# Performance work log

Hardware: AMD Instinct MI355X
Metric: run time of the kernel (lower is better)

The kernel has to match this reference:

```python
import jax, jax.numpy as jnp
import numpy as np

NEG_INF = -10000.0


def setup_inputs() -> dict:
    key = jax.random.key(0)
    ks = jax.random.split(key, 8)
    B, S, H, V, NU, MV = 32, 256, 768, 30522, 5, 4
    f = lambda k, shape, s=1.0: jax.random.normal(k, shape, dtype=jnp.float32) * s
    return dict(
        input_ids=jax.random.randint(ks[0], (B, S), 0, V),
        decoder_inputs=f(ks[1], (B, NU, H)),
        encoder_output=f(ks[2], (B, S, H)),
        hidden=f(ks[3], (1, B, H)),
        embed_weight=f(ks[4], (V, H), 0.02),
        gru_w_ih=f(ks[5], (3 * H, H), 0.02),
        gru_w_hh=f(ks[6], (3 * H, H), 0.02),
        gru_b_ih=jnp.zeros((3 * H,), jnp.float32),
        gru_b_hh=jnp.zeros((3 * H,), jnp.float32),
        wgen_w=f(ks[7], (1, 3 * H), 0.02),
        wgen_b=jnp.zeros((1,), jnp.float32),
        max_value=MV,
    )


def reference(input_ids, decoder_inputs, encoder_output, hidden, embed_weight,
              gru_w_ih, gru_w_hh, gru_b_ih, gru_b_hh, wgen_w, wgen_b, max_value):
    B, S = input_ids.shape
    V, H = embed_weight.shape
    mask = (input_ids == 0)                      # [B,S] pad mask
    rows = jnp.arange(B)[:, None]                # for batched scatter-add

    def gru_cell(x, h):                          # PyTorch GRU, gate order r,z,n
        gi = x @ gru_w_ih.T + gru_b_ih
        gh = h @ gru_w_hh.T + gru_b_hh
        i_r, i_z, i_n = jnp.split(gi, 3, axis=-1)
        h_r, h_z, h_n = jnp.split(gh, 3, axis=-1)
        r = jax.nn.sigmoid(i_r + h_r)
        z = jax.nn.sigmoid(i_z + h_z)
        n = jnp.tanh(i_n + r * h_n)
        return (1.0 - z) * n + z * h

    def inner(carry, _):
        w, h = carry                             # w: [B,H] current input token emb
        h = gru_cell(w, h)                       # [B,H]
        attn_e = jnp.einsum('bsh,bh->bs', encoder_output, h)
        attn_hist = jax.nn.softmax(jnp.where(mask, NEG_INF, attn_e), axis=-1)  # [B,S]
        attn_vocab = jax.nn.softmax(h @ embed_weight.T, axis=-1)               # [B,V]
        context = jnp.einsum('bs,bsh->bh', attn_hist, encoder_output)          # [B,H]
        p_gen = jax.nn.sigmoid(
            jnp.concatenate([w, h, context], axis=-1) @ wgen_w.T + wgen_b)     # [B,1]
        # pointer distribution: scatter attention mass onto vocab ids
        p_ptr = jnp.zeros((B, V), attn_vocab.dtype).at[rows, input_ids].add(attn_hist)
        p_final = p_gen * attn_vocab + (1.0 - p_gen) * p_ptr                   # [B,V]
        w_idx = jnp.argmax(p_final, axis=-1)                                   # greedy
        return (embed_weight[w_idx], h), p_final

    def outer(h, w0):                            # w0: [B,H] slot query embedding
        (_, h), p = jax.lax.scan(inner, (w0, h), None, length=max_value)
        return h, p                              # p: [max_value,B,V]

    h0 = hidden[0]                               # [B,H]
    _, outs = jax.lax.scan(outer, h0, jnp.swapaxes(decoder_inputs, 0, 1))
    # outs: [n_update, max_value, B, V] -> [B, n_update, max_value, V]
    return jnp.transpose(outs, (2, 0, 1, 3))
```

## Files before the change

kernel.cpp:

```cpp
#include <hip/hip_runtime.h>
#include <math.h>

#define B 32
#define S 256
#define H 768
#define V 30522
#define NU 5
#define MV 4
#define NEG_INF -10000.0f

#define VP 30720
#define KSPLIT 4
#define KCH 192
#define KT 32
#define VT 256
#define VPAD 260

__device__ __forceinline__ float sigm(float x){ return 1.0f/(1.0f + expf(-x)); }

__global__ __launch_bounds__(256) void gru_kernel(
    const float* __restrict__ wp, int wstride,
    const float* __restrict__ hin, float* __restrict__ hout,
    float* __restrict__ htr,
    const float* __restrict__ Wih, const float* __restrict__ Whh,
    const float* __restrict__ bih, const float* __restrict__ bhh)
{
    int wid  = blockIdx.x * 4 + (threadIdx.x >> 6);
    int lane = threadIdx.x & 63;
    int j  = wid >> 2;
    int bg = wid & 3;

    float aI0[8], aI1[8], aI2[8], aH0[8], aH1[8], aH2[8];
#pragma unroll
    for (int bb = 0; bb < 8; bb++){ aI0[bb]=aI1[bb]=aI2[bb]=aH0[bb]=aH1[bb]=aH2[bb]=0.f; }

#pragma unroll
    for (int it = 0; it < 3; it++){
        int k = it*256 + lane*4;
        float4 w0 = *(const float4*)(Wih + (size_t)(0*H + j)*H + k);
        float4 w1 = *(const float4*)(Wih + (size_t)(1*H + j)*H + k);
        float4 w2 = *(const float4*)(Wih + (size_t)(2*H + j)*H + k);
        float4 u0 = *(const float4*)(Whh + (size_t)(0*H + j)*H + k);
        float4 u1 = *(const float4*)(Whh + (size_t)(1*H + j)*H + k);
        float4 u2 = *(const float4*)(Whh + (size_t)(2*H + j)*H + k);
#pragma unroll
        for (int bb = 0; bb < 8; bb++){
            int b = bg*8 + bb;
            float4 x = *(const float4*)(wp  + (size_t)b*wstride + k);
            float4 h = *(const float4*)(hin + (size_t)b*H + k);
            aI0[bb] += w0.x*x.x + w0.y*x.y + w0.z*x.z + w0.w*x.w;
            aI1[bb] += w1.x*x.x + w1.y*x.y + w1.z*x.z + w1.w*x.w;
            aI2[bb] += w2.x*x.x + w2.y*x.y + w2.z*x.z + w2.w*x.w;
            aH0[bb] += u0.x*h.x + u0.y*h.y + u0.z*h.z + u0.w*h.w;
            aH1[bb] += u1.x*h.x + u1.y*h.y + u1.z*h.z + u1.w*h.w;
            aH2[bb] += u2.x*h.x + u2.y*h.y + u2.z*h.z + u2.w*h.w;
        }
    }
    float rRZ0[8], rRZ1[8], rIN[8], rHN[8];
#pragma unroll
    for (int bb = 0; bb < 8; bb++){
        rRZ0[bb] = aI0[bb] + aH0[bb];
        rRZ1[bb] = aI1[bb] + aH1[bb];
        rIN[bb]  = aI2[bb];
        rHN[bb]  = aH2[bb];
    }
#pragma unroll
    for (int bb = 0; bb < 8; bb++){
#pragma unroll
        for (int m = 32; m >= 1; m >>= 1){
            rRZ0[bb] += __shfl_xor(rRZ0[bb], m, 64);
            rRZ1[bb] += __shfl_xor(rRZ1[bb], m, 64);
            rIN[bb]  += __shfl_xor(rIN[bb],  m, 64);
            rHN[bb]  += __shfl_xor(rHN[bb],  m, 64);
        }
    }
    if (lane == 0){
        float brz0 = bih[j]     + bhh[j];
        float brz1 = bih[H+j]   + bhh[H+j];
        float bin_ = bih[2*H+j];
        float bhn_ = bhh[2*H+j];
#pragma unroll
        for (int bb = 0; bb < 8; bb++){
            int b = bg*8 + bb;
            float r = sigm(rRZ0[bb] + brz0);
            float z = sigm(rRZ1[bb] + brz1);
            float n = tanhf(rIN[bb] + bin_ + r*(rHN[bb] + bhn_));
            float ho = hin[(size_t)b*H + j];
            float hv = (1.0f - z)*n + z*ho;
            hout[(size_t)b*H + j] = hv;
            htr[(size_t)j*32 + b] = hv;
        }
    }
}

__global__ __launch_bounds__(256) void attn_e_kernel(
    const float* __restrict__ hb, const float* __restrict__ enc,
    float* __restrict__ attnE)
{
    int wid  = blockIdx.x * 4 + (threadIdx.x >> 6);
    int lane = threadIdx.x & 63;
    int b = wid >> 8;
    int s = wid & 255;
    const float* er = enc + ((size_t)b*S + s)*H;
    const float* hr = hb + (size_t)b*H;
    float acc = 0.f;
#pragma unroll
    for (int it = 0; it < 3; it++){
        int k = it*256 + lane*4;
        float4 e4 = *(const float4*)(er + k);
        float4 h4 = *(const float4*)(hr + k);
        acc += e4.x*h4.x + e4.y*h4.y + e4.z*h4.z + e4.w*h4.w;
    }
#pragma unroll
    for (int m = 32; m >= 1; m >>= 1) acc += __shfl_xor(acc, m, 64);
    if (lane == 0) attnE[b*S + s] = acc;
}

__global__ __launch_bounds__(256) void ctx_kernel(
    const float* __restrict__ attnE, const int* __restrict__ ids,
    const float* __restrict__ enc, float* __restrict__ attnH,
    float* __restrict__ ctx)
{
    __shared__ float ah[S];
    __shared__ float red[S];
    int b  = blockIdx.x / 3;
    int kc = blockIdx.x % 3;
    int t  = threadIdx.x;

    float e = attnE[b*S + t];
    if (ids[b*S + t] == 0) e = NEG_INF;
    red[t] = e; __syncthreads();
    for (int s = 128; s > 0; s >>= 1){ if (t < s) red[t] = fmaxf(red[t], red[t+s]); __syncthreads(); }
    float mx = red[0]; __syncthreads();
    float p = expf(e - mx);
    red[t] = p; __syncthreads();
    for (int s = 128; s > 0; s >>= 1){ if (t < s) red[t] += red[t+s]; __syncthreads(); }
    float a = p / red[0];
    ah[t] = a;
    if (kc == 0) attnH[b*S + t] = a;
    __syncthreads();

    int k = kc*256 + t;
    const float* ep = enc + (size_t)b*S*H + k;
    float acc = 0.f;
#pragma unroll 4
    for (int s = 0; s < S; s++) acc += ah[s] * ep[(size_t)s*H];
    ctx[b*H + k] = acc;
}

__global__ __launch_bounds__(256) void logits_kernel(
    const float* __restrict__ E, const float* __restrict__ htr,
    float* __restrict__ part,
    const float* __restrict__ hb, const float* __restrict__ wp, int wstride,
    const float* __restrict__ ctx, const float* __restrict__ wgw,
    const float* __restrict__ wgb, float* __restrict__ pgen)
{
    int t = threadIdx.x;

    if (blockIdx.x == 480){
        int b = t >> 3, sl = t & 7;
        float s = 0.f;
        for (int i = sl; i < 2304; i += 8){
            float xv;
            if (i < 768)        xv = wp[(size_t)b*wstride + i];
            else if (i < 1536)  xv = hb[b*H + (i - 768)];
            else                xv = ctx[b*H + (i - 1536)];
            s += xv * wgw[i];
        }
#pragma unroll
        for (int m = 4; m >= 1; m >>= 1) s += __shfl_xor(s, m, 8);
        if (sl == 0) pgen[b] = sigm(s + wgb[0]);
        return;
    }

    __shared__ float Ets[KT][VPAD];
    int vt = blockIdx.x >> 2;
    int ks = blockIdx.x & 3;
    int v0 = vt * VT;
    int k0 = ks * KCH;

    int wu = __builtin_amdgcn_readfirstlane(t >> 6);
    int l  = t & 63;
    int r  = t >> 3;
    int c4 = t & 7;

    float4 acc[8];
#pragma unroll
    for (int j = 0; j < 8; j++){ acc[j].x=0.f; acc[j].y=0.f; acc[j].z=0.f; acc[j].w=0.f; }

    for (int ph = 0; ph < KCH/KT; ph++){
        int kb = k0 + ph*KT;
        __syncthreads();
#pragma unroll
        for (int p = 0; p < 8; p++){
            int vv = v0 + p*32 + r;
            int vr = vv < V ? vv : V-1;
            float4 e4 = *(const float4*)(E + (size_t)vr*H + kb + c4*4);
            int vloc = p*32 + r;
            Ets[c4*4+0][vloc] = e4.x;
            Ets[c4*4+1][vloc] = e4.y;
            Ets[c4*4+2][vloc] = e4.z;
            Ets[c4*4+3][vloc] = e4.w;
        }
        __syncthreads();
        const float* hkp = htr + (size_t)kb*32 + 8*wu;
#pragma unroll
        for (int k = 0; k < KT; k++){
            float4 e4 = *(const float4*)(&Ets[k][l*4]);
            float h0 = hkp[k*32+0], h1 = hkp[k*32+1], h2 = hkp[k*32+2], h3 = hkp[k*32+3];
            float h4 = hkp[k*32+4], h5 = hkp[k*32+5], h6 = hkp[k*32+6], h7 = hkp[k*32+7];
            acc[0].x += h0*e4.x; acc[0].y += h0*e4.y; acc[0].z += h0*e4.z; acc[0].w += h0*e4.w;
            acc[1].x += h1*e4.x; acc[1].y += h1*e4.y; acc[1].z += h1*e4.z; acc[1].w += h1*e4.w;
            acc[2].x += h2*e4.x; acc[2].y += h2*e4.y; acc[2].z += h2*e4.z; acc[2].w += h2*e4.w;
            acc[3].x += h3*e4.x; acc[3].y += h3*e4.y; acc[3].z += h3*e4.z; acc[3].w += h3*e4.w;
            acc[4].x += h4*e4.x; acc[4].y += h4*e4.y; acc[4].z += h4*e4.z; acc[4].w += h4*e4.w;
            acc[5].x += h5*e4.x; acc[5].y += h5*e4.y; acc[5].z += h5*e4.z; acc[5].w += h5*e4.w;
            acc[6].x += h6*e4.x; acc[6].y += h6*e4.y; acc[6].z += h6*e4.z; acc[6].w += h6*e4.w;
            acc[7].x += h7*e4.x; acc[7].y += h7*e4.y; acc[7].z += h7*e4.z; acc[7].w += h7*e4.w;
        }
    }
    float* pp = part + (size_t)ks*32*VP;
    int v = v0 + l*4;
#pragma unroll
    for (int j = 0; j < 8; j++){
        int b = 8*wu + j;
        *(float4*)(pp + (size_t)b*VP + v) = acc[j];
    }
}

__global__ __launch_bounds__(1024) void vred_kernel(
    const float* __restrict__ part, float* __restrict__ vmax, float* __restrict__ vsum)
{
    __shared__ float red[1024];
    int b = blockIdx.x, t = threadIdx.x;
    float r[30]; int n = 0;
    float mx = -INFINITY;
    for (int i = t; i < V; i += 1024){
        float x = part[(size_t)b*VP + i]
                + part[(size_t)(32+b)*VP + i]
                + part[(size_t)(64+b)*VP + i]
                + part[(size_t)(96+b)*VP + i];
        r[n++] = x;
        mx = fmaxf(mx, x);
    }
    red[t] = mx; __syncthreads();
    for (int s = 512; s > 0; s >>= 1){ if (t < s) red[t] = fmaxf(red[t], red[t+s]); __syncthreads(); }
    mx = red[0]; __syncthreads();
    float sm = 0.f;
    for (int i = 0; i < n; i++) sm += expf(r[i] - mx);
    red[t] = sm; __syncthreads();
    for (int s = 512; s > 0; s >>= 1){ if (t < s) red[t] += red[t+s]; __syncthreads(); }
    if (t == 0){ vmax[b] = mx; vsum[b] = red[0]; }
}

__global__ __launch_bounds__(1024) void final_kernel(
    const float* __restrict__ part, const float* __restrict__ vmax,
    const float* __restrict__ vsum, const float* __restrict__ pgen,
    float* __restrict__ out, int u, int mm)
{
    int b = blockIdx.y;
    int v = blockIdx.x*1024 + threadIdx.x;
    if (v >= V) return;
    float x = part[(size_t)b*VP + v]
            + part[(size_t)(32+b)*VP + v]
            + part[(size_t)(64+b)*VP + v]
            + part[(size_t)(96+b)*VP + v];
    float val = pgen[b] * expf(x - vmax[b]) / vsum[b];
    out[(((size_t)b*NU + u)*MV + mm)*(size_t)V + v] = val;
}

__global__ __launch_bounds__(256) void scatter_kernel(
    const float* __restrict__ attnH, const int* __restrict__ ids,
    const float* __restrict__ pgen, float* __restrict__ out, int u, int mm)
{
    int b = blockIdx.x, s = threadIdx.x;
    int id = ids[b*S + s];
    float val = (1.0f - pgen[b]) * attnH[b*S + s];
    atomicAdd(out + (((size_t)b*NU + u)*MV + mm)*(size_t)V + id, val);
}

__global__ __launch_bounds__(1024) void argmax_kernel(
    const float* __restrict__ out, int u, int mm,
    const float* __restrict__ E, float* __restrict__ wbuf)
{
    __shared__ float rv[1024];
    __shared__ int   ri[1024];
    int b = blockIdx.x, t = threadIdx.x;
    const float* row = out + (((size_t)b*NU + u)*MV + mm)*(size_t)V;
    float bv = -INFINITY; int bi = 0;
    for (int i = t; i < V; i += 1024){
        float x = row[i];
        if (x > bv){ bv = x; bi = i; }
    }
    rv[t] = bv; ri[t] = bi; __syncthreads();
    for (int s = 512; s > 0; s >>= 1){
        if (t < s){
            if (rv[t+s] > rv[t] || (rv[t+s] == rv[t] && ri[t+s] < ri[t])){
                rv[t] = rv[t+s]; ri[t] = ri[t+s];
            }
        }
        __syncthreads();
    }
    int idx = ri[0];
    for (int k = t; k < H; k += 1024) wbuf[b*H + k] = E[(size_t)idx*H + k];
}

extern "C" void kernel_launch(void* const* d_in, const int* in_sizes, int n_in,
                              void* d_out, int out_size, void* d_ws, size_t ws_size,
                              hipStream_t stream)
{
    const int*   ids = (const int*)  d_in[0];
    const float* dec = (const float*)d_in[1];
    const float* enc = (const float*)d_in[2];
    const float* hid = (const float*)d_in[3];
    const float* E   = (const float*)d_in[4];
    const float* Wih = (const float*)d_in[5];
    const float* Whh = (const float*)d_in[6];
    const float* bih = (const float*)d_in[7];
    const float* bhh = (const float*)d_in[8];
    const float* wgw = (const float*)d_in[9];
    const float* wgb = (const float*)d_in[10];
    float* out = (float*)d_out;
    float* ws  = (float*)d_ws;

    float* wbuf    = ws;
    float* hb0     = ws + 24576;
    float* hb1     = ws + 49152;
    float* ctxb    = ws + 73728;
    float* attnE   = ws + 98304;
    float* attnH   = ws + 106496;
    float* htr     = ws + 114688;
    float* pgenb   = ws + 139264;
    float* vmaxb   = ws + 139296;
    float* vsumb   = ws + 139328;
    float* part    = ws + 139360;

    for (int u = 0; u < NU; u++){
        for (int mm = 0; mm < MV; mm++){
            int st = u*MV + mm;
            const float* wp; int wstride;
            if (mm == 0){ wp = dec + (size_t)u*H; wstride = NU*H; }
            else        { wp = wbuf;              wstride = H; }
            const float* hin = (st == 0) ? hid : ((st & 1) ? hb0 : hb1);
            float*      hout = (st & 1) ? hb1 : hb0;

            gru_kernel<<<768, 256, 0, stream>>>(wp, wstride, hin, hout, htr, Wih, Whh, bih, bhh);
            attn_e_kernel<<<2048, 256, 0, stream>>>(hout, enc, attnE);
            ctx_kernel<<<96, 256, 0, stream>>>(attnE, ids, enc, attnH, ctxb);
            logits_kernel<<<481, 256, 0, stream>>>(E, htr, part, hout, wp, wstride, ctxb, wgw, wgb, pgenb);
            vred_kernel<<<32, 1024, 0, stream>>>(part, vmaxb, vsumb);
            final_kernel<<<dim3(30, 32), 1024, 0, stream>>>(part, vmaxb, vsumb, pgenb, out, u, mm);
            scatter_kernel<<<32, 256, 0, stream>>>(attnH, ids, pgenb, out, u, mm);
            if (mm != MV-1)
                argmax_kernel<<<32, 1024, 0, stream>>>(out, u, mm, E, wbuf);
        }
    }
}
```

Measured before the change: 3.417 ms.

## Fuse softmax, scatter and argmax into one kernel; retile logits GEMV

Replaces the vocab reduction, final softmax write, pointer scatter and argmax kernels with one per-row kernel that keeps logits in registers. This avoids re-reading the partial logits and saves several launches per step. The logits kernel moves to 128-wide vocab tiles, stages h in shared memory and computes four batches per thread, doubling the block count. The fused kernel runs only 32 blocks for the output write and argmax, which may limit parallelism.

```diff
diff --git a/kernel.cpp b/kernel.cpp
--- a/kernel.cpp
+++ b/kernel.cpp
@@ -10,11 +10,11 @@
 #define NEG_INF -10000.0f
 
 #define VP 30720
+#define NT 239
+#define VT 128
 #define KSPLIT 4
 #define KCH 192
 #define KT 32
-#define VT 256
-#define VPAD 260
 
 __device__ __forceinline__ float sigm(float x){ return 1.0f/(1.0f + expf(-x)); }
 
@@ -157,7 +157,7 @@
 {
     int t = threadIdx.x;
 
-    if (blockIdx.x == 480){
+    if (blockIdx.x == NT*4){
         int b = t >> 3, sl = t & 7;
         float s = 0.f;
         for (int i = sl; i < 2304; i += 8){
@@ -173,130 +173,135 @@
         return;
     }
 
-    __shared__ float Ets[KT][VPAD];
+    __shared__ float Ets[KT][VT];
+    __shared__ float Hs[KCH][32];
+
     int vt = blockIdx.x >> 2;
     int ks = blockIdx.x & 3;
     int v0 = vt * VT;
     int k0 = ks * KCH;
 
-    int wu = __builtin_amdgcn_readfirstlane(t >> 6);
+#pragma unroll
+    for (int j = 0; j < 6; j++){
+        int idx = t + 256*j;
+        float4 hv = *(const float4*)(htr + (size_t)k0*32 + (size_t)idx*4);
+        *(float4*)((float*)Hs + (size_t)idx*4) = hv;
+    }
+
+    int w  = t >> 6;
     int l  = t & 63;
-    int r  = t >> 3;
-    int c4 = t & 7;
-
-    float4 acc[8];
-#pragma unroll
-    for (int j = 0; j < 8; j++){ acc[j].x=0.f; acc[j].y=0.f; acc[j].z=0.f; acc[j].w=0.f; }
+    int vq = l & 31;
+    int bh = l >> 5;
+    int kq = t & 7;
+    int sr = t >> 3;
+
+    float4 acc[4];
+#pragma unroll
+    for (int j = 0; j < 4; j++){ acc[j].x=0.f; acc[j].y=0.f; acc[j].z=0.f; acc[j].w=0.f; }
 
     for (int ph = 0; ph < KCH/KT; ph++){
         int kb = k0 + ph*KT;
         __syncthreads();
 #pragma unroll
-        for (int p = 0; p < 8; p++){
-            int vv = v0 + p*32 + r;
-            int vr = vv < V ? vv : V-1;
-            float4 e4 = *(const float4*)(E + (size_t)vr*H + kb + c4*4);
-            int vloc = p*32 + r;
-            Ets[c4*4+0][vloc] = e4.x;
-            Ets[c4*4+1][vloc] = e4.y;
-            Ets[c4*4+2][vloc] = e4.z;
-            Ets[c4*4+3][vloc] = e4.w;
+        for (int i = 0; i < 4; i++){
+            int v = sr + 32*i;
+            int vr = v0 + v; if (vr >= V) vr = V-1;
+            float4 e4 = *(const float4*)(E + (size_t)vr*H + kb + 4*kq);
+            Ets[4*kq+0][v] = e4.x;
+            Ets[4*kq+1][v] = e4.y;
+            Ets[4*kq+2][v] = e4.z;
+            Ets[4*kq+3][v] = e4.w;
         }
         __syncthreads();
-        const float* hkp = htr + (size_t)kb*32 + 8*wu;
-#pragma unroll
+        int hbase = 8*w + 4*bh;
+#pragma unroll 4
         for (int k = 0; k < KT; k++){
-            float4 e4 = *(const float4*)(&Ets[k][l*4]);
-            float h0 = hkp[k*32+0], h1 = hkp[k*32+1], h2 = hkp[k*32+2], h3 = hkp[k*32+3];
-            float h4 = hkp[k*32+4], h5 = hkp[k*32+5], h6 = hkp[k*32+6], h7 = hkp[k*32+7];
-            acc[0].x += h0*e4.x; acc[0].y += h0*e4.y; acc[0].z += h0*e4.z; acc[0].w += h0*e4.w;
-            acc[1].x += h1*e4.x; acc[1].y += h1*e4.y; acc[1].z += h1*e4.z; acc[1].w += h1*e4.w;
-            acc[2].x += h2*e4.x; acc[2].y += h2*e4.y; acc[2].z += h2*e4.z; acc[2].w += h2*e4.w;
-            acc[3].x += h3*e4.x; acc[3].y += h3*e4.y; acc[3].z += h3*e4.z; acc[3].w += h3*e4.w;
-            acc[4].x += h4*e4.x; acc[4].y += h4*e4.y; acc[4].z += h4*e4.z; acc[4].w += h4*e4.w;
-            acc[5].x += h5*e4.x; acc[5].y += h5*e4.y; acc[5].z += h5*e4.z; acc[5].w += h5*e4.w;
-            acc[6].x += h6*e4.x; acc[6].y += h6*e4.y; acc[6].z += h6*e4.z; acc[6].w += h6*e4.w;
-            acc[7].x += h7*e4.x; acc[7].y += h7*e4.y; acc[7].z += h7*e4.z; acc[7].w += h7*e4.w;
+            float4 e4 = *(const float4*)(&Ets[k][4*vq]);
+            float4 h4 = *(const float4*)(&Hs[ph*KT + k][hbase]);
+            acc[0].x += h4.x*e4.x; acc[0].y += h4.x*e4.y; acc[0].z += h4.x*e4.z; acc[0].w += h4.x*e4.w;
+            acc[1].x += h4.y*e4.x; acc[1].y += h4.y*e4.y; acc[1].z += h4.y*e4.z; acc[1].w += h4.y*e4.w;
+            acc[2].x += h4.z*e4.x; acc[2].y += h4.z*e4.y; acc[2].z += h4.z*e4.z; acc[2].w += h4.z*e4.w;
+            acc[3].x += h4.w*e4.x; acc[3].y += h4.w*e4.y; acc[3].z += h4.w*e4.z; acc[3].w += h4.w*e4.w;
         }
     }
     float* pp = part + (size_t)ks*32*VP;
-    int v = v0 + l*4;
-#pragma unroll
-    for (int j = 0; j < 8; j++){
-        int b = 8*wu + j;
+    int v = v0 + 4*vq;
+#pragma unroll
+    for (int j = 0; j < 4; j++){
+        int b = 8*w + 4*bh + j;
         *(float4*)(pp + (size_t)b*VP + v) = acc[j];
     }
 }
 
-__global__ __launch_bounds__(1024) void vred_kernel(
-    const float* __restrict__ part, float* __restrict__ vmax, float* __restrict__ vsum)
+__global__ __launch_bounds__(1024) void softmax_fused_kernel(
+    const float* __restrict__ part, const float* __restrict__ pgen,
+    const float* __restrict__ attnH, const int* __restrict__ ids,
+    float* __restrict__ out, const float* __restrict__ E,
+    float* __restrict__ wbuf, int u, int mm)
 {
     __shared__ float red[1024];
+    __shared__ int   ri[1024];
     int b = blockIdx.x, t = threadIdx.x;
-    float r[30]; int n = 0;
+
+    float r[30];
     float mx = -INFINITY;
-    for (int i = t; i < V; i += 1024){
-        float x = part[(size_t)b*VP + i]
-                + part[(size_t)(32+b)*VP + i]
-                + part[(size_t)(64+b)*VP + i]
-                + part[(size_t)(96+b)*VP + i];
-        r[n++] = x;
+#pragma unroll
+    for (int i = 0; i < 30; i++){
+        int v = t + 1024*i;
+        float x = -INFINITY;
+        if (v < V){
+            x = part[(size_t)b*VP + v]
+              + part[(size_t)(32+b)*VP + v]
+              + part[(size_t)(64+b)*VP + v]
+              + part[(size_t)(96+b)*VP + v];
+        }
+        r[i] = x;
         mx = fmaxf(mx, x);
     }
     red[t] = mx; __syncthreads();
     for (int s = 512; s > 0; s >>= 1){ if (t < s) red[t] = fmaxf(red[t], red[t+s]); __syncthreads(); }
     mx = red[0]; __syncthreads();
+
     float sm = 0.f;
-    for (int i = 0; i < n; i++) sm += expf(r[i] - mx);
+#pragma unroll
+    for (int i = 0; i < 30; i++){
+        if (t + 1024*i < V) sm += expf(r[i] - mx);
+    }
     red[t] = sm; __syncthreads();
     for (int s = 512; s > 0; s >>= 1){ if (t < s) red[t] += red[t+s]; __syncthreads(); }
-    if (t == 0){ vmax[b] = mx; vsum[b] = red[0]; }
-}
-
-__global__ __launch_bounds__(1024) void final_kernel(
-    const float* __restrict__ part, const float* __restrict__ vmax,
-    const float* __restrict__ vsum, const float* __restrict__ pgen,
-    float* __restrict__ out, int u, int mm)
-{
-    int b = blockIdx.y;
-    int v = blockIdx.x*1024 + threadIdx.x;
-    if (v >= V) return;
-    float x = part[(size_t)b*VP + v]
-            + part[(size_t)(32+b)*VP + v]
-            + part[(size_t)(64+b)*VP + v]
-            + part[(size_t)(96+b)*VP + v];
-    float val = pgen[b] * expf(x - vmax[b]) / vsum[b];
-    out[(((size_t)b*NU + u)*MV + mm)*(size_t)V + v] = val;
-}
-
-__global__ __launch_bounds__(256) void scatter_kernel(
-    const float* __restrict__ attnH, const int* __restrict__ ids,
-    const float* __restrict__ pgen, float* __restrict__ out, int u, int mm)
-{
-    int b = blockIdx.x, s = threadIdx.x;
-    int id = ids[b*S + s];
-    float val = (1.0f - pgen[b]) * attnH[b*S + s];
-    atomicAdd(out + (((size_t)b*NU + u)*MV + mm)*(size_t)V + id, val);
-}
-
-__global__ __launch_bounds__(1024) void argmax_kernel(
-    const float* __restrict__ out, int u, int mm,
-    const float* __restrict__ E, float* __restrict__ wbuf)
-{
-    __shared__ float rv[1024];
-    __shared__ int   ri[1024];
-    int b = blockIdx.x, t = threadIdx.x;
-    const float* row = out + (((size_t)b*NU + u)*MV + mm)*(size_t)V;
+    float sum = red[0]; __syncthreads();
+
+    float pg  = pgen[b];
+    float scl = pg / sum;
+    float* orow = out + (((size_t)b*NU + u)*MV + mm)*(size_t)V;
+#pragma unroll
+    for (int i = 0; i < 30; i++){
+        int v = t + 1024*i;
+        if (v < V) orow[v] = expf(r[i] - mx) * scl;
+    }
+    __threadfence();
+    __syncthreads();
+    if (t < S){
+        int id = ids[b*S + t];
+        atomicAdd(orow + id, (1.0f - pg) * attnH[b*S + t]);
+    }
+    __threadfence();
+    __syncthreads();
+
     float bv = -INFINITY; int bi = 0;
-    for (int i = t; i < V; i += 1024){
-        float x = row[i];
-        if (x > bv){ bv = x; bi = i; }
-    }
-    rv[t] = bv; ri[t] = bi; __syncthreads();
+#pragma unroll
+    for (int i = 0; i < 30; i++){
+        int v = t + 1024*i;
+        if (v < V){
+            float x = orow[v];
+            if (x > bv){ bv = x; bi = v; }
+        }
+    }
+    red[t] = bv; ri[t] = bi; __syncthreads();
     for (int s = 512; s > 0; s >>= 1){
         if (t < s){
-            if (rv[t+s] > rv[t] || (rv[t+s] == rv[t] && ri[t+s] < ri[t])){
-                rv[t] = rv[t+s]; ri[t] = ri[t+s];
+            if (red[t+s] > red[t] || (red[t+s] == red[t] && ri[t+s] < ri[t])){
+                red[t] = red[t+s]; ri[t] = ri[t+s];
             }
         }
         __syncthreads();
@@ -331,8 +336,6 @@
     float* attnH   = ws + 106496;
     float* htr     = ws + 114688;
     float* pgenb   = ws + 139264;
-    float* vmaxb   = ws + 139296;
-    float* vsumb   = ws + 139328;
     float* part    = ws + 139360;
 
     for (int u = 0; u < NU; u++){
@@ -347,12 +350,8 @@
             gru_kernel<<<768, 256, 0, stream>>>(wp, wstride, hin, hout, htr, Wih, Whh, bih, bhh);
             attn_e_kernel<<<2048, 256, 0, stream>>>(hout, enc, attnE);
             ctx_kernel<<<96, 256, 0, stream>>>(attnE, ids, enc, attnH, ctxb);
-            logits_kernel<<<481, 256, 0, stream>>>(E, htr, part, hout, wp, wstride, ctxb, wgw, wgb, pgenb);
-            vred_kernel<<<32, 1024, 0, stream>>>(part, vmaxb, vsumb);
-            final_kernel<<<dim3(30, 32), 1024, 0, stream>>>(part, vmaxb, vsumb, pgenb, out, u, mm);
-            scatter_kernel<<<32, 256, 0, stream>>>(attnH, ids, pgenb, out, u, mm);
-            if (mm != MV-1)
-                argmax_kernel<<<32, 1024, 0, stream>>>(out, u, mm, E, wbuf);
-        }
-    }
-}
+            logits_kernel<<<NT*4+1, 256, 0, stream>>>(E, htr, part, hout, wp, wstride, ctxb, wgw, wgb, pgenb);
+            softmax_fused_kernel<<<32, 1024, 0, stream>>>(part, pgenb, attnH, ids, out, E, wbuf, u, mm);
+        }
+    }
+}
```

Result: slower. 3.823 ms (+11.9%).

## Restructure vocab logits with 6-way K-split, prefetch, and fused softmax+scatter

Applied to the files above, without the earlier changes.

The logits kernel now splits K six ways (720 blocks), stages the hidden-state slice in shared memory, and register-prefetches the next embedding tile while computing the current one. The vocab reduction is split into 8 chunks per batch row, producing partial max/sum and a reduced logit buffer. The final kernel merges the partial softmax stats, writes float4 outputs, and performs the pointer scatter-add itself, which removes a separate kernel launch. These changes aim to raise parallelism and overlap global loads with FMA work. The cost is more partial-sum traffic and an extra intermediate buffer.

```diff
diff --git a/kernel.cpp b/kernel.cpp
--- a/kernel.cpp
+++ b/kernel.cpp
@@ -10,11 +10,12 @@
 #define NEG_INF -10000.0f
 
 #define VP 30720
-#define KSPLIT 4
-#define KCH 192
-#define KT 32
+#define VTILES 120
 #define VT 256
-#define VPAD 260
+#define KSPL 6
+#define KCH 128
+#define KT 16
+#define NPH (KCH/KT)
 
 __device__ __forceinline__ float sigm(float x){ return 1.0f/(1.0f + expf(-x)); }
 
@@ -157,7 +158,7 @@
 {
     int t = threadIdx.x;
 
-    if (blockIdx.x == 480){
+    if (blockIdx.x == VTILES*KSPL){
         int b = t >> 3, sl = t & 7;
         float s = 0.f;
         for (int i = sl; i < 2304; i += 8){
@@ -173,110 +174,152 @@
         return;
     }
 
-    __shared__ float Ets[KT][VPAD];
-    int vt = blockIdx.x >> 2;
-    int ks = blockIdx.x & 3;
+    __shared__ float Ets[KT][VT];
+    __shared__ float Hs[KCH][32];
+
+    int vt = blockIdx.x / KSPL;
+    int ks = blockIdx.x % KSPL;
     int v0 = vt * VT;
     int k0 = ks * KCH;
 
-    int wu = __builtin_amdgcn_readfirstlane(t >> 6);
+    {
+        const float4* src = (const float4*)(htr + (size_t)k0*32);
+        float4* dst = (float4*)&Hs[0][0];
+#pragma unroll
+        for (int i = 0; i < 4; i++) dst[t + 256*i] = src[t + 256*i];
+    }
+
+    int q  = t & 3;
+    int vs = t >> 2;
+    int w  = t >> 6;
     int l  = t & 63;
-    int r  = t >> 3;
-    int c4 = t & 7;
+
+    float4 pre[4];
+#pragma unroll
+    for (int a = 0; a < 4; a++){
+        int vr = v0 + vs + 64*a; if (vr >= V) vr = V-1;
+        pre[a] = *(const float4*)(E + (size_t)vr*H + k0 + 4*q);
+    }
 
     float4 acc[8];
 #pragma unroll
     for (int j = 0; j < 8; j++){ acc[j].x=0.f; acc[j].y=0.f; acc[j].z=0.f; acc[j].w=0.f; }
 
-    for (int ph = 0; ph < KCH/KT; ph++){
-        int kb = k0 + ph*KT;
+    for (int ph = 0; ph < NPH; ph++){
         __syncthreads();
 #pragma unroll
-        for (int p = 0; p < 8; p++){
-            int vv = v0 + p*32 + r;
-            int vr = vv < V ? vv : V-1;
-            float4 e4 = *(const float4*)(E + (size_t)vr*H + kb + c4*4);
-            int vloc = p*32 + r;
-            Ets[c4*4+0][vloc] = e4.x;
-            Ets[c4*4+1][vloc] = e4.y;
-            Ets[c4*4+2][vloc] = e4.z;
-            Ets[c4*4+3][vloc] = e4.w;
+        for (int a = 0; a < 4; a++){
+            int vloc = vs + 64*a;
+            Ets[4*q+0][vloc] = pre[a].x;
+            Ets[4*q+1][vloc] = pre[a].y;
+            Ets[4*q+2][vloc] = pre[a].z;
+            Ets[4*q+3][vloc] = pre[a].w;
         }
         __syncthreads();
-        const float* hkp = htr + (size_t)kb*32 + 8*wu;
+        if (ph + 1 < NPH){
+            int kn = k0 + (ph+1)*KT;
+#pragma unroll
+            for (int a = 0; a < 4; a++){
+                int vr = v0 + vs + 64*a; if (vr >= V) vr = V-1;
+                pre[a] = *(const float4*)(E + (size_t)vr*H + kn + 4*q);
+            }
+        }
 #pragma unroll
         for (int k = 0; k < KT; k++){
-            float4 e4 = *(const float4*)(&Ets[k][l*4]);
-            float h0 = hkp[k*32+0], h1 = hkp[k*32+1], h2 = hkp[k*32+2], h3 = hkp[k*32+3];
-            float h4 = hkp[k*32+4], h5 = hkp[k*32+5], h6 = hkp[k*32+6], h7 = hkp[k*32+7];
-            acc[0].x += h0*e4.x; acc[0].y += h0*e4.y; acc[0].z += h0*e4.z; acc[0].w += h0*e4.w;
-            acc[1].x += h1*e4.x; acc[1].y += h1*e4.y; acc[1].z += h1*e4.z; acc[1].w += h1*e4.w;
-            acc[2].x += h2*e4.x; acc[2].y += h2*e4.y; acc[2].z += h2*e4.z; acc[2].w += h2*e4.w;
-            acc[3].x += h3*e4.x; acc[3].y += h3*e4.y; acc[3].z += h3*e4.z; acc[3].w += h3*e4.w;
-            acc[4].x += h4*e4.x; acc[4].y += h4*e4.y; acc[4].z += h4*e4.z; acc[4].w += h4*e4.w;
-            acc[5].x += h5*e4.x; acc[5].y += h5*e4.y; acc[5].z += h5*e4.z; acc[5].w += h5*e4.w;
-            acc[6].x += h6*e4.x; acc[6].y += h6*e4.y; acc[6].z += h6*e4.z; acc[6].w += h6*e4.w;
-            acc[7].x += h7*e4.x; acc[7].y += h7*e4.y; acc[7].z += h7*e4.z; acc[7].w += h7*e4.w;
+            float4 e4 = *(const float4*)(&Ets[k][4*l]);
+            const float* hp = &Hs[ph*KT + k][8*w];
+            float4 hA = *(const float4*)(hp);
+            float4 hB = *(const float4*)(hp + 4);
+            acc[0].x += hA.x*e4.x; acc[0].y += hA.x*e4.y; acc[0].z += hA.x*e4.z; acc[0].w += hA.x*e4.w;
+            acc[1].x += hA.y*e4.x; acc[1].y += hA.y*e4.y; acc[1].z += hA.y*e4.z; acc[1].w += hA.y*e4.w;
+            acc[2].x += hA.z*e4.x; acc[2].y += hA.z*e4.y; acc[2].z += hA.z*e4.z; acc[2].w += hA.z*e4.w;
+            acc[3].x += hA.w*e4.x; acc[3].y += hA.w*e4.y; acc[3].z += hA.w*e4.z; acc[3].w += hA.w*e4.w;
+            acc[4].x += hB.x*e4.x; acc[4].y += hB.x*e4.y; acc[4].z += hB.x*e4.z; acc[4].w += hB.x*e4.w;
+            acc[5].x += hB.y*e4.x; acc[5].y += hB.y*e4.y; acc[5].z += hB.y*e4.z; acc[5].w += hB.y*e4.w;
+            acc[6].x += hB.z*e4.x; acc[6].y += hB.z*e4.y; acc[6].z += hB.z*e4.z; acc[6].w += hB.z*e4.w;
+            acc[7].x += hB.w*e4.x; acc[7].y += hB.w*e4.y; acc[7].z += hB.w*e4.z; acc[7].w += hB.w*e4.w;
         }
     }
     float* pp = part + (size_t)ks*32*VP;
-    int v = v0 + l*4;
+    int v = v0 + 4*l;
 #pragma unroll
     for (int j = 0; j < 8; j++){
-        int b = 8*wu + j;
+        int b = 8*w + j;
         *(float4*)(pp + (size_t)b*VP + v) = acc[j];
     }
 }
 
-__global__ __launch_bounds__(1024) void vred_kernel(
-    const float* __restrict__ part, float* __restrict__ vmax, float* __restrict__ vsum)
-{
-    __shared__ float red[1024];
-    int b = blockIdx.x, t = threadIdx.x;
-    float r[30]; int n = 0;
+#define VCH 3816
+__global__ __launch_bounds__(256) void vred1_kernel(
+    const float* __restrict__ part, float* __restrict__ lsum,
+    float* __restrict__ pm, float* __restrict__ ps)
+{
+    __shared__ float red[256];
+    int b = blockIdx.x >> 3, c = blockIdx.x & 7;
+    int t = threadIdx.x;
+    int vlo = c*VCH;
+    int vhi = vlo + VCH; if (vhi > V) vhi = V;
+
+    float r[15]; int n = 0;
     float mx = -INFINITY;
-    for (int i = t; i < V; i += 1024){
-        float x = part[(size_t)b*VP + i]
-                + part[(size_t)(32+b)*VP + i]
-                + part[(size_t)(64+b)*VP + i]
-                + part[(size_t)(96+b)*VP + i];
+    for (int v = vlo + t; v < vhi; v += 256){
+        float x = 0.f;
+#pragma unroll
+        for (int s = 0; s < KSPL; s++) x += part[(size_t)(32*s + b)*VP + v];
+        lsum[(size_t)b*VP + v] = x;
         r[n++] = x;
         mx = fmaxf(mx, x);
     }
     red[t] = mx; __syncthreads();
-    for (int s = 512; s > 0; s >>= 1){ if (t < s) red[t] = fmaxf(red[t], red[t+s]); __syncthreads(); }
+    for (int s = 128; s > 0; s >>= 1){ if (t < s) red[t] = fmaxf(red[t], red[t+s]); __syncthreads(); }
     mx = red[0]; __syncthreads();
     float sm = 0.f;
     for (int i = 0; i < n; i++) sm += expf(r[i] - mx);
     red[t] = sm; __syncthreads();
-    for (int s = 512; s > 0; s >>= 1){ if (t < s) red[t] += red[t+s]; __syncthreads(); }
-    if (t == 0){ vmax[b] = mx; vsum[b] = red[0]; }
-}
-
-__global__ __launch_bounds__(1024) void final_kernel(
-    const float* __restrict__ part, const float* __restrict__ vmax,
-    const float* __restrict__ vsum, const float* __restrict__ pgen,
+    for (int s = 128; s > 0; s >>= 1){ if (t < s) red[t] += red[t+s]; __syncthreads(); }
+    if (t == 0){ pm[b*8 + c] = mx; ps[b*8 + c] = red[0]; }
+}
+
+__global__ __launch_bounds__(256) void final_kernel(
+    const float* __restrict__ lsum, const float* __restrict__ pm,
+    const float* __restrict__ ps, const float* __restrict__ pgen,
+    const float* __restrict__ attnH, const int* __restrict__ ids,
     float* __restrict__ out, int u, int mm)
 {
-    int b = blockIdx.y;
-    int v = blockIdx.x*1024 + threadIdx.x;
-    if (v >= V) return;
-    float x = part[(size_t)b*VP + v]
-            + part[(size_t)(32+b)*VP + v]
-            + part[(size_t)(64+b)*VP + v]
-            + part[(size_t)(96+b)*VP + v];
-    float val = pgen[b] * expf(x - vmax[b]) / vsum[b];
-    out[(((size_t)b*NU + u)*MV + mm)*(size_t)V + v] = val;
-}
-
-__global__ __launch_bounds__(256) void scatter_kernel(
-    const float* __restrict__ attnH, const int* __restrict__ ids,
-    const float* __restrict__ pgen, float* __restrict__ out, int u, int mm)
-{
-    int b = blockIdx.x, s = threadIdx.x;
-    int id = ids[b*S + s];
-    float val = (1.0f - pgen[b]) * attnH[b*S + s];
-    atomicAdd(out + (((size_t)b*NU + u)*MV + mm)*(size_t)V + id, val);
+    int b = blockIdx.x / 30;
+    int c = blockIdx.x % 30;
+    int t = threadIdx.x;
+
+    float M = -INFINITY;
+#pragma unroll
+    for (int i = 0; i < 8; i++) M = fmaxf(M, pm[b*8+i]);
+    float Ssum = 0.f;
+#pragma unroll
+    for (int i = 0; i < 8; i++) Ssum += ps[b*8+i] * expf(pm[b*8+i] - M);
+    float pg  = pgen[b];
+    float scl = pg / Ssum;
+
+    int vlo = c*1024;
+    float* orow = out + (((size_t)b*NU + u)*MV + mm)*(size_t)V;
+    int v = vlo + 4*t;
+    float4 x = *(const float4*)(lsum + (size_t)b*VP + v);
+    if (v + 3 < V){
+        float4 o;
+        o.x = expf(x.x - M)*scl; o.y = expf(x.y - M)*scl;
+        o.z = expf(x.z - M)*scl; o.w = expf(x.w - M)*scl;
+        *(float4*)(orow + v) = o;
+    } else {
+        if (v+0 < V) orow[v+0] = expf(x.x - M)*scl;
+        if (v+1 < V) orow[v+1] = expf(x.y - M)*scl;
+        if (v+2 < V) orow[v+2] = expf(x.z - M)*scl;
+        if (v+3 < V) orow[v+3] = expf(x.w - M)*scl;
+    }
+    __threadfence();
+    __syncthreads();
+    int id = ids[b*S + t];
+    if (id >= vlo && id < vlo + 1024){
+        atomicAdd(orow + id, (1.0f - pg) * attnH[b*S + t]);
+    }
 }
 
 __global__ __launch_bounds__(1024) void argmax_kernel(
@@ -331,9 +374,10 @@
     float* attnH   = ws + 106496;
     float* htr     = ws + 114688;
     float* pgenb   = ws + 139264;
-    float* vmaxb   = ws + 139296;
-    float* vsumb   = ws + 139328;
-    float* part    = ws + 139360;
+    float* pm      = ws + 139296;
+    float* psb     = ws + 139552;
+    float* lsum    = ws + 139808;
+    float* part    = ws + 1122848;
 
     for (int u = 0; u < NU; u++){
         for (int mm = 0; mm < MV; mm++){
@@ -347,10 +391,9 @@
             gru_kernel<<<768, 256, 0, stream>>>(wp, wstride, hin, hout, htr, Wih, Whh, bih, bhh);
             attn_e_kernel<<<2048, 256, 0, stream>>>(hout, enc, attnE);
             ctx_kernel<<<96, 256, 0, stream>>>(attnE, ids, enc, attnH, ctxb);
-            logits_kernel<<<481, 256, 0, stream>>>(E, htr, part, hout, wp, wstride, ctxb, wgw, wgb, pgenb);
-            vred_kernel<<<32, 1024, 0, stream>>>(part, vmaxb, vsumb);
-            final_kernel<<<dim3(30, 32), 1024, 0, stream>>>(part, vmaxb, vsumb, pgenb, out, u, mm);
-            scatter_kernel<<<32, 256, 0, stream>>>(attnH, ids, pgenb, out, u, mm);
+            logits_kernel<<<VTILES*KSPL+1, 256, 0, stream>>>(E, htr, part, hout, wp, wstride, ctxb, wgw, wgb, pgenb);
+            vred1_kernel<<<256, 256, 0, stream>>>(part, lsum, pm, psb);
+            final_kernel<<<960, 256, 0, stream>>>(lsum, pm, psb, pgenb, attnH, ids, out, u, mm);
             if (mm != MV-1)
                 argmax_kernel<<<32, 1024, 0, stream>>>(out, u, mm, E, wbuf);
         }
```

Result: slower. 4.866 ms (+42.4%).
